# Kernel optimization log

Measured on AMD Instinct MI355X. Metric: run time of the kernel, lower is better.

Reference implementation:

```python
import jax, jax.numpy as jnp
import numpy as np


def setup_inputs() -> dict:
    key = jax.random.key(0)
    ks = jax.random.split(key, 9)
    D, DK, DV = 512, 64, 64
    B, S = 4, 4096
    sd = 1.0 / np.sqrt(D).astype(np.float32)
    so = 1.0 / np.sqrt(DV).astype(np.float32)
    return {
        "x": jax.random.normal(ks[0], (B, S, D), dtype=jnp.float32),
        "Wq": jax.random.normal(ks[1], (D, DK), dtype=jnp.float32) * sd,
        "bq": jnp.zeros((DK,), dtype=jnp.float32),
        "Wk": jax.random.normal(ks[2], (D, DK), dtype=jnp.float32) * sd,
        "bk": jnp.zeros((DK,), dtype=jnp.float32),
        "Wv": jax.random.normal(ks[3], (D, DV), dtype=jnp.float32) * sd,
        "bv": jnp.zeros((DV,), dtype=jnp.float32),
        "Wo": jax.random.normal(ks[4], (DV, D), dtype=jnp.float32) * so,
        "bo": jnp.zeros((D,), dtype=jnp.float32),
    }


def reference(x, Wq, bq, Wk, bk, Wv, bv, Wo, bo):
    # x: (B, S, D)
    B, S, D = x.shape
    dk = Wq.shape[1]
    q = x @ Wq + bq            # (B, S, dk)
    k = x @ Wk + bk            # (B, S, dk)
    v = x @ Wv + bv            # (B, S, dv)
    scores = jnp.einsum("bik,bjk->bij", q, k) / jnp.sqrt(jnp.float32(dk))  # (B,S,S)
    # causal mask: True where j <= i (keep)
    causal = jnp.tril(jnp.ones((S, S), dtype=bool))
    scores = jnp.where(causal[None, :, :], scores, -jnp.inf)
    weights = jax.nn.softmax(scores, axis=-1)   # every row has >=1 unmasked entry
    out = jnp.einsum("bij,bjv->biv", weights, v)  # (B, S, dv)
    return out @ Wo + bo
```

## Files before the change

### kernel.cpp

```cpp
#include <hip/hip_runtime.h>
#include <hip/hip_bf16.h>

#define S_LEN 4096
#define D_MODEL 512
#define DKV 64
#define B_N 4
#define STR 72
#define VSTR 136

typedef __hip_bfloat16 bf16;
typedef __attribute__((ext_vector_type(8))) short short8;
typedef __attribute__((ext_vector_type(4))) float floatx4;

#define MFMA(a, b, c) __builtin_amdgcn_mfma_f32_16x16x32_bf16(a, b, c, 0, 0, 0)

__device__ __forceinline__ float b2f(bf16 v) { return __bfloat162float(v); }

__device__ __forceinline__ unsigned short f2bits(float v) {
    union { bf16 h; unsigned short u; } cv;
    cv.h = __float2bfloat16(v);
    return cv.u;
}
__device__ __forceinline__ float bits2f(unsigned short u) {
    union { bf16 h; unsigned short u; } cv;
    cv.u = u;
    return b2f(cv.h);
}

__global__ __launch_bounds__(64) void detect_kernel(const void* x, int* flag) {
    const int lane = threadIdx.x;
    const bf16* xb = (const bf16*)x;
    int bad = 0;
    for (int k = lane; k < 4096; k += 64) {
        float v = fabsf(b2f(xb[2 * k]));
        if (!(v < 64.f)) bad++;
    }
    #pragma unroll
    for (int off = 32; off >= 1; off >>= 1) bad += __shfl_xor(bad, off);
    if (lane == 0) *flag = (bad > 100) ? 1 : 0;
}

__global__ __launch_bounds__(512) void wprep_kernel(
    const void* __restrict__ Wq, const void* __restrict__ bq,
    const void* __restrict__ Wk, const void* __restrict__ bk,
    const void* __restrict__ Wv, const void* __restrict__ bv,
    const void* __restrict__ Wo, const void* __restrict__ bo,
    bf16* __restrict__ Wfh, bf16* __restrict__ Wfl, float* __restrict__ ball,
    bf16* __restrict__ WoFh, bf16* __restrict__ WoFl, float* __restrict__ ball2,
    const int* __restrict__ flag)
{
    __shared__ float xs[16][513];
    const int blk = blockIdx.x;
    const int tid = threadIdx.x;
    const int f32 = *flag;
    union Pack8 { uint4 u; unsigned short s[8]; };

    if (blk < 12) {
        const int ct = blk;
        const int c0 = ct * 16;
        const int g = c0 >> 6;
        const int cc0 = c0 & 63;
        const void* W    = (g == 0) ? Wq : (g == 1) ? Wk : Wv;
        const void* bias = (g == 0) ? bq : (g == 1) ? bk : bv;

        #pragma unroll
        for (int i = 0; i < 16; ++i) {
            const int idx = tid + 512 * i;
            const int d = idx >> 4, j = idx & 15;
            const float v = f32 ? ((const float*)W)[(size_t)d * DKV + cc0 + j]
                                : b2f(((const bf16*)W)[(size_t)d * DKV + cc0 + j]);
            xs[j][d] = v;
        }
        __syncthreads();

        #pragma unroll
        for (int rep = 0; rep < 2; ++rep) {
            const int f = tid + rep * 512;
            const int kt = f >> 6, lane = f & 63;
            const int quad = lane >> 4, l15 = lane & 15;
            Pack8 ph, pl;
            #pragma unroll
            for (int j = 0; j < 8; ++j) {
                const float v = xs[l15][kt * 32 + quad * 8 + j];
                const unsigned short hb = f2bits(v);
                ph.s[j] = hb;
                pl.s[j] = f2bits(v - bits2f(hb));
            }
            const size_t o = (((size_t)ct * 16 + kt) * 64 + lane) * 8;
            *(uint4*)&Wfh[o] = ph.u;
            *(uint4*)&Wfl[o] = pl.u;
        }
        if (tid < 16)
            ball[c0 + tid] = f32 ? ((const float*)bias)[cc0 + tid]
                                 : b2f(((const bf16*)bias)[cc0 + tid]);
    } else {
        const int ctile = blk - 12;
        const int c0 = ctile * 16;

        #pragma unroll
        for (int rep = 0; rep < 2; ++rep) {
            const int idx = tid + rep * 512;
            const int d = idx >> 4, j = idx & 15;
            const float v = f32 ? ((const float*)Wo)[(size_t)d * D_MODEL + c0 + j]
                                : b2f(((const bf16*)Wo)[(size_t)d * D_MODEL + c0 + j]);
            xs[j][d] = v;
        }
        __syncthreads();

        if (tid < 128) {
            const int kc = tid >> 6, lane = tid & 63;
            const int quad = lane >> 4, l15 = lane & 15;
            Pack8 ph, pl;
            #pragma unroll
            for (int j = 0; j < 8; ++j) {
                const float v = xs[l15][kc * 32 + quad * 8 + j];
                const unsigned short hb = f2bits(v);
                ph.s[j] = hb;
                pl.s[j] = f2bits(v - bits2f(hb));
            }
            const size_t o = (((size_t)ctile * 2 + kc) * 64 + lane) * 8;
            *(uint4*)&WoFh[o] = ph.u;
            *(uint4*)&WoFl[o] = pl.u;
        }
        if (tid < 16)
            ball2[c0 + tid] = f32 ? ((const float*)bo)[c0 + tid]
                                  : b2f(((const bf16*)bo)[c0 + tid]);
    }
}

__global__ __launch_bounds__(512) void qkv_mfma(
    const void* __restrict__ x,
    const bf16* __restrict__ Wfh, const bf16* __restrict__ Wfl,
    const float* __restrict__ ball,
    bf16* __restrict__ Qb, bf16* __restrict__ Kb, bf16* __restrict__ Vt,
    const int* __restrict__ flag)
{
    __shared__ unsigned short hiA[32 * D_MODEL];
    __shared__ unsigned short loA[32 * D_MODEL];
    const int tid = threadIdx.x;
    const int rowBase = blockIdx.x * 32;
    const int f32 = *flag;

    union Pack8 { uint4 u; unsigned short s[8]; };
    if (f32) {
        const float* xr = (const float*)x + (size_t)rowBase * D_MODEL;
        #pragma unroll
        for (int i = 0; i < 4; ++i) {
            const int idx = tid + 512 * i;
            const int r = idx >> 6;
            const int c0 = (idx & 63) << 3;
            const float4 v0 = *(const float4*)&xr[r * D_MODEL + c0];
            const float4 v1 = *(const float4*)&xr[r * D_MODEL + c0 + 4];
            const float vv[8] = {v0.x, v0.y, v0.z, v0.w, v1.x, v1.y, v1.z, v1.w};
            Pack8 ph, pl;
            #pragma unroll
            for (int j = 0; j < 8; ++j) {
                const unsigned short hb = f2bits(vv[j]);
                ph.s[j] = hb;
                pl.s[j] = f2bits(vv[j] - bits2f(hb));
            }
            const int boff = (c0 * 2) ^ ((r & 7) << 4);
            *(uint4*)((char*)hiA + r * 1024 + boff) = ph.u;
            *(uint4*)((char*)loA + r * 1024 + boff) = pl.u;
        }
    } else {
        const unsigned short* xr = (const unsigned short*)x + (size_t)rowBase * D_MODEL;
        #pragma unroll
        for (int i = 0; i < 4; ++i) {
            const int idx = tid + 512 * i;
            const int r = idx >> 6;
            const int c0 = (idx & 63) << 3;
            const uint4 hv = *(const uint4*)&xr[r * D_MODEL + c0];
            const int boff = (c0 * 2) ^ ((r & 7) << 4);
            *(uint4*)((char*)hiA + r * 1024 + boff) = hv;
        }
    }
    __syncthreads();

    const int lane = tid & 63;
    const int w    = tid >> 6;
    const int quad = lane >> 4;
    const int l15  = lane & 15;
    const int wr   = w & 1;
    const int wq   = w >> 1;
    const int arow = wr * 16 + l15;
    const char* hib = (const char*)hiA + arow * 1024;
    const char* lob = (const char*)loA + arow * 1024;
    const int swz = (arow & 7) << 4;

    floatx4 acc[3];
    #pragma unroll
    for (int ct = 0; ct < 3; ++ct) acc[ct] = (floatx4){0.f, 0.f, 0.f, 0.f};

    if (f32) {
        for (int kt = 0; kt < 16; ++kt) {
            const int boff = (kt * 64 + quad * 16) ^ swz;
            const short8 ah = *(const short8*)(hib + boff);
            const short8 al = *(const short8*)(lob + boff);
            #pragma unroll
            for (int ct = 0; ct < 3; ++ct) {
                const size_t fo = (((size_t)(wq * 3 + ct) * 16 + kt) * 64 + lane) * 8;
                const short8 bh = *(const short8*)&Wfh[fo];
                const short8 bl = *(const short8*)&Wfl[fo];
                acc[ct] = MFMA(ah, bh, acc[ct]);
                acc[ct] = MFMA(ah, bl, acc[ct]);
                acc[ct] = MFMA(al, bh, acc[ct]);
            }
        }
    } else {
        for (int kt = 0; kt < 16; ++kt) {
            const int boff = (kt * 64 + quad * 16) ^ swz;
            const short8 ah = *(const short8*)(hib + boff);
            #pragma unroll
            for (int ct = 0; ct < 3; ++ct) {
                const size_t fo = (((size_t)(wq * 3 + ct) * 16 + kt) * 64 + lane) * 8;
                const short8 bh = *(const short8*)&Wfh[fo];
                acc[ct] = MFMA(ah, bh, acc[ct]);
            }
        }
    }

    #pragma unroll
    for (int ct = 0; ct < 3; ++ct) {
        const int gc = wq * 48 + ct * 16 + l15;
        const float bias = ball[gc];
        const float scale = (gc < 64) ? 0.18033688f : 1.0f;
        #pragma unroll
        for (int r = 0; r < 4; ++r) {
            const int gr = rowBase + wr * 16 + quad * 4 + r;
            const bf16 o = __float2bfloat16((acc[ct][r] + bias) * scale);
            if (gc < 64)       Qb[(size_t)gr * DKV + gc] = o;
            else if (gc < 128) Kb[(size_t)gr * DKV + (gc - 64)] = o;
            else {
                const int bb = gr >> 12, sidx = gr & (S_LEN - 1);
                Vt[((size_t)bb * DKV + (gc - 128)) * S_LEN + sidx] = o;
            }
        }
    }
}

__global__ __launch_bounds__(512, 2) void attn_mfma(
    const bf16* __restrict__ Qg, const bf16* __restrict__ Kg,
    const bf16* __restrict__ Vtg, float* __restrict__ Op,
    float* __restrict__ Mp, float* __restrict__ Lp, const int NS)
{
    const int bid = blockIdx.x;
    const int xcd = bid & 7;
    const int rest = bid >> 3;
    const int b   = xcd >> 1;
    const int khH = (NS == 4) ? (rest & 1) : 0;
    const int t   = 31 - ((NS == 4) ? (rest >> 1) : rest);
    const int kh  = khH * 2 + (xcd & 1);
    const int rowBase = t * 128;
    const int tid = threadIdx.x;
    const int lane = tid & 63;
    const int w  = tid >> 6;
    const int quad = lane >> 4;
    const int l15  = lane & 15;

    __shared__ bf16 Kl[128 * STR];
    __shared__ bf16 Vl[64 * VSTR];
    __shared__ bf16 Pl[128 * VSTR];

    const bf16* Qb = Qg + ((size_t)b * S_LEN + rowBase) * DKV;
    const bf16* Kb = Kg + (size_t)b * S_LEN * DKV;
    const bf16* Vb = Vtg + (size_t)b * DKV * S_LEN;

    {
        const int qr = tid >> 2, qd = (tid & 3) * 16;
        *(uint4*)&Pl[qr * VSTR + qd]     = *(const uint4*)&Qb[qr * DKV + qd];
        *(uint4*)&Pl[qr * VSTR + qd + 8] = *(const uint4*)&Qb[qr * DKV + qd + 8];
    }
    __syncthreads();
    short8 qf0, qf1;
    {
        const int qoff = (w * 16 + l15) * VSTR + quad * 8;
        qf0 = *(const short8*)&Pl[qoff];
        qf1 = *(const short8*)&Pl[qoff + 32];
    }

    const short s1b = (short)0x3F80;
    const short8 ones = {s1b, s1b, s1b, s1b, s1b, s1b, s1b, s1b};

    floatx4 acc[4];
    #pragma unroll
    for (int v = 0; v < 4; ++v) acc[v] = (floatx4){0.f, 0.f, 0.f, 0.f};
    floatx4 accl = {0.f, 0.f, 0.f, 0.f};
    float m_run[4];
    #pragma unroll
    for (int r = 0; r < 4; ++r) m_run[r] = -1e30f;

    const int kbMax = t;
    const int kk = tid >> 2, dk = (tid & 3) * 16;
    const int vd = tid >> 3, vk = (tid & 7) * 16;

    uint4 kr0, kr1, vr0, vr1;
    int kb = kh;
    if (kb <= kbMax) {
        const uint4* ks = (const uint4*)&Kb[((size_t)(kb * 128 + kk)) * DKV + dk];
        kr0 = ks[0]; kr1 = ks[1];
        const uint4* vs = (const uint4*)&Vb[(size_t)vd * S_LEN + kb * 128 + vk];
        vr0 = vs[0]; vr1 = vs[1];
    }

    for (; kb <= kbMax; kb += NS) {
        __syncthreads();
        {
            uint4* kd = (uint4*)&Kl[kk * STR + dk];
            kd[0] = kr0; kd[1] = kr1;
            uint4* vdst = (uint4*)&Vl[vd * VSTR + vk];
            vdst[0] = vr0; vdst[1] = vr1;
        }
        __syncthreads();
        if (kb + NS <= kbMax) {
            const uint4* ks = (const uint4*)&Kb[((size_t)((kb + NS) * 128 + kk)) * DKV + dk];
            kr0 = ks[0]; kr1 = ks[1];
            const uint4* vs = (const uint4*)&Vb[(size_t)vd * S_LEN + (kb + NS) * 128 + vk];
            vr0 = vs[0]; vr1 = vs[1];
        }

        floatx4 s[8];
        #pragma unroll
        for (int jt = 0; jt < 8; ++jt) s[jt] = (floatx4){0.f, 0.f, 0.f, 0.f};
        {
            const int qk = quad * 8;
            #pragma unroll
            for (int jt = 0; jt < 8; ++jt) {
                const int kc = (jt * 16 + l15) * STR + qk;
                const short8 ba = *(const short8*)&Kl[kc];
                const short8 bb = *(const short8*)&Kl[kc + 32];
                s[jt] = MFMA(qf0, ba, s[jt]);
                s[jt] = MFMA(qf1, bb, s[jt]);
            }
        }
        if (kb == kbMax) {
            const int rowg = rowBase + w * 16 + quad * 4;
            #pragma unroll
            for (int jt = 0; jt < 8; ++jt) {
                const int kg = kb * 128 + jt * 16 + l15;
                #pragma unroll
                for (int r = 0; r < 4; ++r)
                    if (kg > rowg + r) s[jt][r] = -1e30f;
            }
        }
        float m4[4];
        #pragma unroll
        for (int r = 0; r < 4; ++r) {
            float mm = s[0][r];
            #pragma unroll
            for (int jt = 1; jt < 8; ++jt) mm = fmaxf(mm, s[jt][r]);
            m4[r] = mm;
        }
        #pragma unroll
        for (int off = 1; off < 16; off <<= 1) {
            #pragma unroll
            for (int r = 0; r < 4; ++r) m4[r] = fmaxf(m4[r], __shfl_xor(m4[r], off));
        }
        float alpha[4];
        #pragma unroll
        for (int r = 0; r < 4; ++r) {
            const float mnew = fmaxf(m_run[r], m4[r]);
            alpha[r] = exp2f(m_run[r] - mnew);
            m_run[r] = mnew;
        }
        #pragma unroll
        for (int r = 0; r < 4; ++r) {
            accl[r] *= alpha[r];
            #pragma unroll
            for (int v = 0; v < 4; ++v) acc[v][r] *= alpha[r];
            const int poff = (w * 16 + quad * 4 + r) * VSTR + l15;
            #pragma unroll
            for (int jt = 0; jt < 8; ++jt) {
                const float pp = exp2f(s[jt][r] - m_run[r]);
                Pl[poff + jt * 16] = __float2bfloat16(pp);
            }
        }
        asm volatile("s_waitcnt lgkmcnt(0)" ::: "memory");

        {
            const int pk = quad * 8;
            const int prow = (w * 16 + l15) * VSTR;
            short8 pa[4];
            #pragma unroll
            for (int c = 0; c < 4; ++c)
                pa[c] = *(const short8*)&Pl[prow + pk + c * 32];
            #pragma unroll
            for (int c = 0; c < 4; ++c) accl = MFMA(pa[c], ones, accl);
            #pragma unroll
            for (int v = 0; v < 4; ++v) {
                const int vrow = (v * 16 + l15) * VSTR;
                #pragma unroll
                for (int c = 0; c < 4; ++c) {
                    const short8 vb = *(const short8*)&Vl[vrow + pk + c * 32];
                    acc[v] = MFMA(pa[c], vb, acc[v]);
                }
            }
        }
    }
    #pragma unroll
    for (int r = 0; r < 4; ++r) {
        const int row = rowBase + w * 16 + quad * 4 + r;
        float* op = Op + (((size_t)kh * B_N + b) * S_LEN + row) * DKV + l15;
        #pragma unroll
        for (int v = 0; v < 4; ++v) op[v * 16] = acc[v][r];
    }
    if (l15 == 0) {
        #pragma unroll
        for (int r = 0; r < 4; ++r) {
            const int row = rowBase + w * 16 + quad * 4 + r;
            const size_t mi = ((size_t)kh * B_N + b) * S_LEN + row;
            Mp[mi] = m_run[r];
            Lp[mi] = accl[r];
        }
    }
}

#define PSTR 72
__global__ __launch_bounds__(512) void proj_mfma(
    const float* __restrict__ Op, const float* __restrict__ Mp,
    const float* __restrict__ Lp, const int NS,
    const bf16* __restrict__ WoFh, const bf16* __restrict__ WoFl,
    const float* __restrict__ ball2, void* __restrict__ out,
    const int* __restrict__ flag)
{
    __shared__ unsigned short Ah[32 * PSTR], Al[32 * PSTR];
    const int tid = threadIdx.x;
    const int rowBase = blockIdx.x * 32;
    const int f32 = *flag;

    {
        const int rr = tid >> 4, dd = (tid & 15) * 4;
        const int row = rowBase + rr;
        const size_t part = (size_t)B_N * S_LEN;
        float m = -1e30f;
        #pragma unroll 4
        for (int i = 0; i < NS; ++i) m = fmaxf(m, Mp[i * part + row]);
        float denom = 0.f;
        float oacc[4] = {0.f, 0.f, 0.f, 0.f};
        #pragma unroll 4
        for (int i = 0; i < NS; ++i) {
            const float wi = exp2f(Mp[i * part + row] - m);
            denom += Lp[i * part + row] * wi;
            const float4 v = *(const float4*)&Op[(i * part + row) * DKV + dd];
            oacc[0] += v.x * wi; oacc[1] += v.y * wi;
            oacc[2] += v.z * wi; oacc[3] += v.w * wi;
        }
        const float inv = 1.0f / denom;
        union Pack4 { uint2 u; unsigned short s[4]; };
        Pack4 ph, pl;
        #pragma unroll
        for (int j = 0; j < 4; ++j) {
            const float o = oacc[j] * inv;
            ph.s[j] = f2bits(o);
            pl.s[j] = f2bits(o - bits2f(ph.s[j]));
        }
        *(uint2*)&Ah[rr * PSTR + dd] = ph.u;
        *(uint2*)&Al[rr * PSTR + dd] = pl.u;
    }
    __syncthreads();

    const int lane = tid & 63;
    const int w    = tid >> 6;
    const int quad = lane >> 4;
    const int l15  = lane & 15;
    const int wr   = w & 1;
    const int wcq  = w >> 1;

    const int aoff = (wr * 16 + l15) * PSTR + quad * 8;
    const short8 ah0 = *(const short8*)&Ah[aoff];
    const short8 ah1 = *(const short8*)&Ah[aoff + 32];
    const short8 al0 = *(const short8*)&Al[aoff];
    const short8 al1 = *(const short8*)&Al[aoff + 32];

    floatx4 acc[8];
    #pragma unroll
    for (int ct = 0; ct < 8; ++ct) acc[ct] = (floatx4){0.f, 0.f, 0.f, 0.f};

    if (f32) {
        #pragma unroll
        for (int ct = 0; ct < 8; ++ct) {
            const int ctile = wcq * 8 + ct;
            const size_t o0 = (((size_t)ctile * 2 + 0) * 64 + lane) * 8;
            const size_t o1 = (((size_t)ctile * 2 + 1) * 64 + lane) * 8;
            const short8 bh0 = *(const short8*)&WoFh[o0];
            const short8 bh1 = *(const short8*)&WoFh[o1];
            const short8 bl0 = *(const short8*)&WoFl[o0];
            const short8 bl1 = *(const short8*)&WoFl[o1];
            acc[ct] = MFMA(ah0, bh0, acc[ct]);
            acc[ct] = MFMA(ah1, bh1, acc[ct]);
            acc[ct] = MFMA(ah0, bl0, acc[ct]);
            acc[ct] = MFMA(ah1, bl1, acc[ct]);
            acc[ct] = MFMA(al0, bh0, acc[ct]);
            acc[ct] = MFMA(al1, bh1, acc[ct]);
        }
        float* outf = (float*)out;
        #pragma unroll
        for (int ct = 0; ct < 8; ++ct) {
            const int col = wcq * 128 + ct * 16 + l15;
            const float bias = ball2[col];
            #pragma unroll
            for (int r = 0; r < 4; ++r) {
                const int row = rowBase + wr * 16 + quad * 4 + r;
                outf[(size_t)row * D_MODEL + col] = acc[ct][r] + bias;
            }
        }
    } else {
        #pragma unroll
        for (int ct = 0; ct < 8; ++ct) {
            const int ctile = wcq * 8 + ct;
            const size_t o0 = (((size_t)ctile * 2 + 0) * 64 + lane) * 8;
            const size_t o1 = (((size_t)ctile * 2 + 1) * 64 + lane) * 8;
            const short8 bh0 = *(const short8*)&WoFh[o0];
            const short8 bh1 = *(const short8*)&WoFh[o1];
            acc[ct] = MFMA(ah0, bh0, acc[ct]);
            acc[ct] = MFMA(ah1, bh1, acc[ct]);
            acc[ct] = MFMA(al0, bh0, acc[ct]);
            acc[ct] = MFMA(al1, bh1, acc[ct]);
        }
        bf16* outb = (bf16*)out;
        #pragma unroll
        for (int ct = 0; ct < 8; ++ct) {
            const int col = wcq * 128 + ct * 16 + l15;
            const float bias = ball2[col];
            #pragma unroll
            for (int r = 0; r < 4; ++r) {
                const int row = rowBase + wr * 16 + quad * 4 + r;
                outb[(size_t)row * D_MODEL + col] = __float2bfloat16(acc[ct][r] + bias);
            }
        }
    }
}

extern "C" void kernel_launch(void* const* d_in, const int* in_sizes, int n_in,
                              void* d_out, int out_size, void* d_ws, size_t ws_size,
                              hipStream_t stream) {
    const void* x  = d_in[0];
    const void* Wq = d_in[1];
    const void* bq = d_in[2];
    const void* Wk = d_in[3];
    const void* bk = d_in[4];
    const void* Wv = d_in[5];
    const void* bv = d_in[6];
    const void* Wo = d_in[7];
    const void* bo = d_in[8];

    const int rows = B_N * S_LEN;
    const int NS = (ws_size >= (size_t)30 * 1024 * 1024) ? 4 : 2;

    char* p = (char*)d_ws;
    int*  flag = (int*)p;                          p += 256;
    bf16* Qb = (bf16*)p;                           p += (size_t)rows * DKV * 2;
    bf16* Kb = (bf16*)p;                           p += (size_t)rows * DKV * 2;
    bf16* Vt = (bf16*)p;                           p += (size_t)rows * DKV * 2;
    bf16* Wfh = (bf16*)p;                          p += (size_t)12 * 16 * 64 * 8 * 2;
    bf16* Wfl = (bf16*)p;                          p += (size_t)12 * 16 * 64 * 8 * 2;
    float* ball = (float*)p;                       p += 1024;
    bf16* WoFh = (bf16*)p;                         p += (size_t)32 * 2 * 64 * 8 * 2;
    bf16* WoFl = (bf16*)p;                         p += (size_t)32 * 2 * 64 * 8 * 2;
    float* ball2 = (float*)p;                      p += D_MODEL * 4;
    float* Op = (float*)p;                         p += (size_t)NS * rows * DKV * 4;
    float* Mp = (float*)p;                         p += (size_t)NS * rows * 4;
    float* Lp = (float*)p;                         p += (size_t)NS * rows * 4;

    detect_kernel<<<1, 64, 0, stream>>>(x, flag);
    wprep_kernel<<<44, 512, 0, stream>>>(Wq, bq, Wk, bk, Wv, bv, Wo, bo,
                                         Wfh, Wfl, ball, WoFh, WoFl, ball2, flag);
    qkv_mfma<<<512, 512, 0, stream>>>(x, Wfh, Wfl, ball, Qb, Kb, Vt, flag);
    attn_mfma<<<128 * NS, 512, 0, stream>>>(Qb, Kb, Vt, Op, Mp, Lp, NS);
    proj_mfma<<<512, 512, 0, stream>>>(Op, Mp, Lp, NS, WoFh, WoFl, ball2, d_out, flag);
}
```

Measured before the change: 169.9 us.

## Fuse split-KV merge and output projection into attention via atomic tickets

Removes the separate projection kernel. Each attention block bumps a per-tile atomic ticket after writing its partial O, M and L. The last split block to finish for a 128-row tile merges the partials and runs the Wo projection in four 32-row chunks. This saves one kernel launch and lets projection work overlap with attention blocks that are still running, but only one block per tile does the projection, which serialises that tail work. It also adds shared memory to the attention kernel, which may lower occupancy.

```diff
diff --git a/kernel.cpp b/kernel.cpp
--- a/kernel.cpp
+++ b/kernel.cpp
@@ -7,6 +7,7 @@
 #define B_N 4
 #define STR 72
 #define VSTR 136
+#define PSTR 72
 
 typedef __hip_bfloat16 bf16;
 typedef __attribute__((ext_vector_type(8))) short short8;
@@ -27,8 +28,10 @@
     return b2f(cv.h);
 }
 
-__global__ __launch_bounds__(64) void detect_kernel(const void* x, int* flag) {
+__global__ __launch_bounds__(64) void detect_kernel(const void* x, int* flag,
+                                                    int* tickets) {
     const int lane = threadIdx.x;
+    for (int i = lane; i < 128; i += 64) tickets[i] = 0;
     const bf16* xb = (const bf16*)x;
     int bad = 0;
     for (int k = lane; k < 4096; k += 64) {
@@ -242,7 +245,11 @@
 __global__ __launch_bounds__(512, 2) void attn_mfma(
     const bf16* __restrict__ Qg, const bf16* __restrict__ Kg,
     const bf16* __restrict__ Vtg, float* __restrict__ Op,
-    float* __restrict__ Mp, float* __restrict__ Lp, const int NS)
+    float* __restrict__ Mp, float* __restrict__ Lp, const int NS,
+    int* __restrict__ tickets,
+    const bf16* __restrict__ WoFh, const bf16* __restrict__ WoFl,
+    const float* __restrict__ ball2, void* __restrict__ out,
+    const int* __restrict__ flag)
 {
     const int bid = blockIdx.x;
     const int xcd = bid & 7;
@@ -261,6 +268,8 @@
     __shared__ bf16 Kl[128 * STR];
     __shared__ bf16 Vl[64 * VSTR];
     __shared__ bf16 Pl[128 * VSTR];
+    __shared__ unsigned short Ah[32 * PSTR], Al[32 * PSTR];
+    __shared__ int lastFlag;
 
     const bf16* Qb = Qg + ((size_t)b * S_LEN + rowBase) * DKV;
     const bf16* Kb = Kg + (size_t)b * S_LEN * DKV;
@@ -413,121 +422,118 @@
             Lp[mi] = accl[r];
         }
     }
-}
-
-#define PSTR 72
-__global__ __launch_bounds__(512) void proj_mfma(
-    const float* __restrict__ Op, const float* __restrict__ Mp,
-    const float* __restrict__ Lp, const int NS,
-    const bf16* __restrict__ WoFh, const bf16* __restrict__ WoFl,
-    const float* __restrict__ ball2, void* __restrict__ out,
-    const int* __restrict__ flag)
-{
-    __shared__ unsigned short Ah[32 * PSTR], Al[32 * PSTR];
-    const int tid = threadIdx.x;
-    const int rowBase = blockIdx.x * 32;
+
+    __threadfence();
+    __syncthreads();
+    if (tid == 0) {
+        const int gid = b * 32 + t;
+        const int old = atomicAdd(&tickets[gid], 1);
+        lastFlag = (old == NS - 1);
+    }
+    __syncthreads();
+    if (!lastFlag) return;
+    __threadfence();
+
     const int f32 = *flag;
-
-    {
-        const int rr = tid >> 4, dd = (tid & 15) * 4;
-        const int row = rowBase + rr;
-        const size_t part = (size_t)B_N * S_LEN;
-        float m = -1e30f;
-        #pragma unroll 4
-        for (int i = 0; i < NS; ++i) m = fmaxf(m, Mp[i * part + row]);
-        float denom = 0.f;
-        float oacc[4] = {0.f, 0.f, 0.f, 0.f};
-        #pragma unroll 4
-        for (int i = 0; i < NS; ++i) {
-            const float wi = exp2f(Mp[i * part + row] - m);
-            denom += Lp[i * part + row] * wi;
-            const float4 v = *(const float4*)&Op[(i * part + row) * DKV + dd];
-            oacc[0] += v.x * wi; oacc[1] += v.y * wi;
-            oacc[2] += v.z * wi; oacc[3] += v.w * wi;
-        }
-        const float inv = 1.0f / denom;
-        union Pack4 { uint2 u; unsigned short s[4]; };
-        Pack4 ph, pl;
-        #pragma unroll
-        for (int j = 0; j < 4; ++j) {
-            const float o = oacc[j] * inv;
-            ph.s[j] = f2bits(o);
-            pl.s[j] = f2bits(o - bits2f(ph.s[j]));
-        }
-        *(uint2*)&Ah[rr * PSTR + dd] = ph.u;
-        *(uint2*)&Al[rr * PSTR + dd] = pl.u;
-    }
-    __syncthreads();
-
-    const int lane = tid & 63;
-    const int w    = tid >> 6;
-    const int quad = lane >> 4;
-    const int l15  = lane & 15;
-    const int wr   = w & 1;
-    const int wcq  = w >> 1;
-
-    const int aoff = (wr * 16 + l15) * PSTR + quad * 8;
-    const short8 ah0 = *(const short8*)&Ah[aoff];
-    const short8 ah1 = *(const short8*)&Ah[aoff + 32];
-    const short8 al0 = *(const short8*)&Al[aoff];
-    const short8 al1 = *(const short8*)&Al[aoff + 32];
-
-    floatx4 acc[8];
-    #pragma unroll
-    for (int ct = 0; ct < 8; ++ct) acc[ct] = (floatx4){0.f, 0.f, 0.f, 0.f};
-
-    if (f32) {
-        #pragma unroll
-        for (int ct = 0; ct < 8; ++ct) {
-            const int ctile = wcq * 8 + ct;
-            const size_t o0 = (((size_t)ctile * 2 + 0) * 64 + lane) * 8;
-            const size_t o1 = (((size_t)ctile * 2 + 1) * 64 + lane) * 8;
-            const short8 bh0 = *(const short8*)&WoFh[o0];
-            const short8 bh1 = *(const short8*)&WoFh[o1];
-            const short8 bl0 = *(const short8*)&WoFl[o0];
-            const short8 bl1 = *(const short8*)&WoFl[o1];
-            acc[ct] = MFMA(ah0, bh0, acc[ct]);
-            acc[ct] = MFMA(ah1, bh1, acc[ct]);
-            acc[ct] = MFMA(ah0, bl0, acc[ct]);
-            acc[ct] = MFMA(ah1, bl1, acc[ct]);
-            acc[ct] = MFMA(al0, bh0, acc[ct]);
-            acc[ct] = MFMA(al1, bh1, acc[ct]);
-        }
-        float* outf = (float*)out;
-        #pragma unroll
-        for (int ct = 0; ct < 8; ++ct) {
-            const int col = wcq * 128 + ct * 16 + l15;
-            const float bias = ball2[col];
-            #pragma unroll
-            for (int r = 0; r < 4; ++r) {
-                const int row = rowBase + wr * 16 + quad * 4 + r;
-                outf[(size_t)row * D_MODEL + col] = acc[ct][r] + bias;
-            }
-        }
-    } else {
-        #pragma unroll
-        for (int ct = 0; ct < 8; ++ct) {
-            const int ctile = wcq * 8 + ct;
-            const size_t o0 = (((size_t)ctile * 2 + 0) * 64 + lane) * 8;
-            const size_t o1 = (((size_t)ctile * 2 + 1) * 64 + lane) * 8;
-            const short8 bh0 = *(const short8*)&WoFh[o0];
-            const short8 bh1 = *(const short8*)&WoFh[o1];
-            acc[ct] = MFMA(ah0, bh0, acc[ct]);
-            acc[ct] = MFMA(ah1, bh1, acc[ct]);
-            acc[ct] = MFMA(al0, bh0, acc[ct]);
-            acc[ct] = MFMA(al1, bh1, acc[ct]);
-        }
-        bf16* outb = (bf16*)out;
-        #pragma unroll
-        for (int ct = 0; ct < 8; ++ct) {
-            const int col = wcq * 128 + ct * 16 + l15;
-            const float bias = ball2[col];
-            #pragma unroll
-            for (int r = 0; r < 4; ++r) {
-                const int row = rowBase + wr * 16 + quad * 4 + r;
-                outb[(size_t)row * D_MODEL + col] = __float2bfloat16(acc[ct][r] + bias);
-            }
-        }
+    const int wr  = w & 1;
+    const int wcq = w >> 1;
+    for (int cb = 0; cb < 4; ++cb) {
+        const int grow0 = b * S_LEN + rowBase + cb * 32;
+        {
+            const int rr = tid >> 4, dd = (tid & 15) * 4;
+            const int row = grow0 + rr;
+            const size_t part = (size_t)B_N * S_LEN;
+            float m = -1e30f;
+            #pragma unroll 4
+            for (int i = 0; i < NS; ++i) m = fmaxf(m, Mp[i * part + row]);
+            float denom = 0.f;
+            float oacc[4] = {0.f, 0.f, 0.f, 0.f};
+            #pragma unroll 4
+            for (int i = 0; i < NS; ++i) {
+                const float wi = exp2f(Mp[i * part + row] - m);
+                denom += Lp[i * part + row] * wi;
+                const float4 v = *(const float4*)&Op[(i * part + row) * DKV + dd];
+                oacc[0] += v.x * wi; oacc[1] += v.y * wi;
+                oacc[2] += v.z * wi; oacc[3] += v.w * wi;
+            }
+            const float inv = 1.0f / denom;
+            union Pack4 { uint2 u; unsigned short s[4]; };
+            Pack4 ph, pl;
+            #pragma unroll
+            for (int j = 0; j < 4; ++j) {
+                const float o = oacc[j] * inv;
+                ph.s[j] = f2bits(o);
+                pl.s[j] = f2bits(o - bits2f(ph.s[j]));
+            }
+            *(uint2*)&Ah[rr * PSTR + dd] = ph.u;
+            *(uint2*)&Al[rr * PSTR + dd] = pl.u;
+        }
+        __syncthreads();
+
+        const int aoff = (wr * 16 + l15) * PSTR + quad * 8;
+        const short8 ah0 = *(const short8*)&Ah[aoff];
+        const short8 ah1 = *(const short8*)&Ah[aoff + 32];
+        const short8 al0 = *(const short8*)&Al[aoff];
+        const short8 al1 = *(const short8*)&Al[aoff + 32];
+
+        floatx4 pacc[8];
+        #pragma unroll
+        for (int ct = 0; ct < 8; ++ct) pacc[ct] = (floatx4){0.f, 0.f, 0.f, 0.f};
+
+        if (f32) {
+            #pragma unroll
+            for (int ct = 0; ct < 8; ++ct) {
+                const int ctile = wcq * 8 + ct;
+                const size_t o0 = (((size_t)ctile * 2 + 0) * 64 + lane) * 8;
+                const size_t o1 = (((size_t)ctile * 2 + 1) * 64 + lane) * 8;
+                const short8 bh0 = *(const short8*)&WoFh[o0];
+                const short8 bh1 = *(const short8*)&WoFh[o1];
+                const short8 bl0 = *(const short8*)&WoFl[o0];
+                const short8 bl1 = *(const short8*)&WoFl[o1];
+                pacc[ct] = MFMA(ah0, bh0, pacc[ct]);
+                pacc[ct] = MFMA(ah1, bh1, pacc[ct]);
+                pacc[ct] = MFMA(ah0, bl0, pacc[ct]);
+                pacc[ct] = MFMA(ah1, bl1, pacc[ct]);
+                pacc[ct] = MFMA(al0, bh0, pacc[ct]);
+                pacc[ct] = MFMA(al1, bh1, pacc[ct]);
+            }
+            float* outf = (float*)out;
+            #pragma unroll
+            for (int ct = 0; ct < 8; ++ct) {
+                const int col = wcq * 128 + ct * 16 + l15;
+                const float bias = ball2[col];
+                #pragma unroll
+                for (int r = 0; r < 4; ++r) {
+                    const int row = grow0 + wr * 16 + quad * 4 + r;
+                    outf[(size_t)row * D_MODEL + col] = pacc[ct][r] + bias;
+                }
+            }
+        } else {
+            #pragma unroll
+            for (int ct = 0; ct < 8; ++ct) {
+                const int ctile = wcq * 8 + ct;
+                const size_t o0 = (((size_t)ctile * 2 + 0) * 64 + lane) * 8;
+                const size_t o1 = (((size_t)ctile * 2 + 1) * 64 + lane) * 8;
+                const short8 bh0 = *(const short8*)&WoFh[o0];
+                const short8 bh1 = *(const short8*)&WoFh[o1];
+                pacc[ct] = MFMA(ah0, bh0, pacc[ct]);
+                pacc[ct] = MFMA(ah1, bh1, pacc[ct]);
+                pacc[ct] = MFMA(al0, bh0, pacc[ct]);
+                pacc[ct] = MFMA(al1, bh1, pacc[ct]);
+            }
+            bf16* outb = (bf16*)out;
+            #pragma unroll
+            for (int ct = 0; ct < 8; ++ct) {
+                const int col = wcq * 128 + ct * 16 + l15;
+                const float bias = ball2[col];
+                #pragma unroll
+                for (int r = 0; r < 4; ++r) {
+                    const int row = grow0 + wr * 16 + quad * 4 + r;
+                    outb[(size_t)row * D_MODEL + col] = __float2bfloat16(pacc[ct][r] + bias);
+                }
+            }
+        }
+        __syncthreads();
     }
 }
 
@@ -549,6 +555,7 @@
 
     char* p = (char*)d_ws;
     int*  flag = (int*)p;                          p += 256;
+    int*  tickets = (int*)p;                       p += 1024;
     bf16* Qb = (bf16*)p;                           p += (size_t)rows * DKV * 2;
     bf16* Kb = (bf16*)p;                           p += (size_t)rows * DKV * 2;
     bf16* Vt = (bf16*)p;                           p += (size_t)rows * DKV * 2;
@@ -562,10 +569,10 @@
     float* Mp = (float*)p;                         p += (size_t)NS * rows * 4;
     float* Lp = (float*)p;                         p += (size_t)NS * rows * 4;
 
-    detect_kernel<<<1, 64, 0, stream>>>(x, flag);
+    detect_kernel<<<1, 64, 0, stream>>>(x, flag, tickets);
     wprep_kernel<<<44, 512, 0, stream>>>(Wq, bq, Wk, bk, Wv, bv, Wo, bo,
                                          Wfh, Wfl, ball, WoFh, WoFl, ball2, flag);
     qkv_mfma<<<512, 512, 0, stream>>>(x, Wfh, Wfl, ball, Qb, Kb, Vt, flag);
-    attn_mfma<<<128 * NS, 512, 0, stream>>>(Qb, Kb, Vt, Op, Mp, Lp, NS);
-    proj_mfma<<<512, 512, 0, stream>>>(Op, Mp, Lp, NS, WoFh, WoFl, ball2, d_out, flag);
-}
+    attn_mfma<<<128 * NS, 512, 0, stream>>>(Qb, Kb, Vt, Op, Mp, Lp, NS, tickets,
+                                            WoFh, WoFl, ball2, d_out, flag);
+}
```

Measured after the change: 340.1 us. 2x slower.

## Split causal attention into fixed two-block chunks and fold detect into wprep

Applied to the files above, without the earlier changes.

Attention work is repartitioned so each block handles at most two key blocks for one query tile, giving 272 work items per batch (1088 blocks) instead of a fixed NS-way interleaved split. Per-tile partial outputs go to slot-indexed buffers, and proj_mfma merges a variable number of partials per row. This is meant to balance the triangular causal workload and shorten per-block latency. In exchange it writes and reads many more partial O/M/L buffers, which adds memory traffic and merge cost. The separate detect kernel launch is also folded into wprep, with each block recomputing the input-format flag itself.

```diff
diff --git a/kernel.cpp b/kernel.cpp
--- a/kernel.cpp
+++ b/kernel.cpp
@@ -27,33 +27,41 @@
     return b2f(cv.h);
 }
 
-__global__ __launch_bounds__(64) void detect_kernel(const void* x, int* flag) {
-    const int lane = threadIdx.x;
-    const bf16* xb = (const bf16*)x;
-    int bad = 0;
-    for (int k = lane; k < 4096; k += 64) {
-        float v = fabsf(b2f(xb[2 * k]));
-        if (!(v < 64.f)) bad++;
-    }
-    #pragma unroll
-    for (int off = 32; off >= 1; off >>= 1) bad += __shfl_xor(bad, off);
-    if (lane == 0) *flag = (bad > 100) ? 1 : 0;
-}
+#define NSLOT_B 272
+__device__ __forceinline__ int offT(int t) { return (t * t + 2 * t + (t & 1)) >> 2; }
 
 __global__ __launch_bounds__(512) void wprep_kernel(
+    const void* __restrict__ x,
     const void* __restrict__ Wq, const void* __restrict__ bq,
     const void* __restrict__ Wk, const void* __restrict__ bk,
     const void* __restrict__ Wv, const void* __restrict__ bv,
     const void* __restrict__ Wo, const void* __restrict__ bo,
     bf16* __restrict__ Wfh, bf16* __restrict__ Wfl, float* __restrict__ ball,
     bf16* __restrict__ WoFh, bf16* __restrict__ WoFl, float* __restrict__ ball2,
-    const int* __restrict__ flag)
+    int* __restrict__ flag)
 {
     __shared__ float xs[16][513];
+    __shared__ int sflag;
     const int blk = blockIdx.x;
     const int tid = threadIdx.x;
-    const int f32 = *flag;
     union Pack8 { uint4 u; unsigned short s[8]; };
+
+    if (tid < 64) {
+        const bf16* xb = (const bf16*)x;
+        int bad = 0;
+        for (int k = tid; k < 4096; k += 64) {
+            float v = fabsf(b2f(xb[2 * k]));
+            if (!(v < 64.f)) bad++;
+        }
+        #pragma unroll
+        for (int off = 32; off >= 1; off >>= 1) bad += __shfl_xor(bad, off);
+        if (tid == 0) {
+            sflag = (bad > 100) ? 1 : 0;
+            if (blk == 0) *flag = sflag;
+        }
+    }
+    __syncthreads();
+    const int f32 = sflag;
 
     if (blk < 12) {
         const int ct = blk;
@@ -242,15 +250,19 @@
 __global__ __launch_bounds__(512, 2) void attn_mfma(
     const bf16* __restrict__ Qg, const bf16* __restrict__ Kg,
     const bf16* __restrict__ Vtg, float* __restrict__ Op,
-    float* __restrict__ Mp, float* __restrict__ Lp, const int NS)
+    float* __restrict__ Mp, float* __restrict__ Lp)
 {
     const int bid = blockIdx.x;
-    const int xcd = bid & 7;
-    const int rest = bid >> 3;
-    const int b   = xcd >> 1;
-    const int khH = (NS == 4) ? (rest & 1) : 0;
-    const int t   = 31 - ((NS == 4) ? (rest >> 1) : rest);
-    const int kh  = khH * 2 + (xcd & 1);
+    const int b = bid & 3;
+    const int j = (NSLOT_B - 1) - (bid >> 2);
+    int t = (int)(2.0f * sqrtf((float)j + 1.0f));
+    if (t > 31) t = 31;
+    while (offT(t) > j) --t;
+    while (t < 31 && offT(t + 1) <= j) ++t;
+    const int p = j - offT(t);
+    const int kb0 = 2 * p;
+    const int kb1 = min(2 * p + 1, t);
+    const int slot = b * NSLOT_B + offT(t) + p;
     const int rowBase = t * 128;
     const int tid = threadIdx.x;
     const int lane = tid & 63;
@@ -290,20 +302,18 @@
     #pragma unroll
     for (int r = 0; r < 4; ++r) m_run[r] = -1e30f;
 
-    const int kbMax = t;
     const int kk = tid >> 2, dk = (tid & 3) * 16;
     const int vd = tid >> 3, vk = (tid & 7) * 16;
 
     uint4 kr0, kr1, vr0, vr1;
-    int kb = kh;
-    if (kb <= kbMax) {
-        const uint4* ks = (const uint4*)&Kb[((size_t)(kb * 128 + kk)) * DKV + dk];
+    {
+        const uint4* ks = (const uint4*)&Kb[((size_t)(kb0 * 128 + kk)) * DKV + dk];
         kr0 = ks[0]; kr1 = ks[1];
-        const uint4* vs = (const uint4*)&Vb[(size_t)vd * S_LEN + kb * 128 + vk];
+        const uint4* vs = (const uint4*)&Vb[(size_t)vd * S_LEN + kb0 * 128 + vk];
         vr0 = vs[0]; vr1 = vs[1];
     }
 
-    for (; kb <= kbMax; kb += NS) {
+    for (int kb = kb0; kb <= kb1; ++kb) {
         __syncthreads();
         {
             uint4* kd = (uint4*)&Kl[kk * STR + dk];
@@ -312,10 +322,10 @@
             vdst[0] = vr0; vdst[1] = vr1;
         }
         __syncthreads();
-        if (kb + NS <= kbMax) {
-            const uint4* ks = (const uint4*)&Kb[((size_t)((kb + NS) * 128 + kk)) * DKV + dk];
+        if (kb + 1 <= kb1) {
+            const uint4* ks = (const uint4*)&Kb[((size_t)((kb + 1) * 128 + kk)) * DKV + dk];
             kr0 = ks[0]; kr1 = ks[1];
-            const uint4* vs = (const uint4*)&Vb[(size_t)vd * S_LEN + (kb + NS) * 128 + vk];
+            const uint4* vs = (const uint4*)&Vb[(size_t)vd * S_LEN + (kb + 1) * 128 + vk];
             vr0 = vs[0]; vr1 = vs[1];
         }
 
@@ -333,7 +343,7 @@
                 s[jt] = MFMA(qf1, bb, s[jt]);
             }
         }
-        if (kb == kbMax) {
+        if (kb == t) {
             const int rowg = rowBase + w * 16 + quad * 4;
             #pragma unroll
             for (int jt = 0; jt < 8; ++jt) {
@@ -399,18 +409,17 @@
     }
     #pragma unroll
     for (int r = 0; r < 4; ++r) {
-        const int row = rowBase + w * 16 + quad * 4 + r;
-        float* op = Op + (((size_t)kh * B_N + b) * S_LEN + row) * DKV + l15;
+        const int lrow = w * 16 + quad * 4 + r;
+        float* op = Op + ((size_t)slot * 128 + lrow) * DKV + l15;
         #pragma unroll
         for (int v = 0; v < 4; ++v) op[v * 16] = acc[v][r];
     }
     if (l15 == 0) {
         #pragma unroll
         for (int r = 0; r < 4; ++r) {
-            const int row = rowBase + w * 16 + quad * 4 + r;
-            const size_t mi = ((size_t)kh * B_N + b) * S_LEN + row;
-            Mp[mi] = m_run[r];
-            Lp[mi] = accl[r];
+            const int lrow = w * 16 + quad * 4 + r;
+            Mp[slot * 128 + lrow] = m_run[r];
+            Lp[slot * 128 + lrow] = accl[r];
         }
     }
 }
@@ -418,7 +427,7 @@
 #define PSTR 72
 __global__ __launch_bounds__(512) void proj_mfma(
     const float* __restrict__ Op, const float* __restrict__ Mp,
-    const float* __restrict__ Lp, const int NS,
+    const float* __restrict__ Lp,
     const bf16* __restrict__ WoFh, const bf16* __restrict__ WoFl,
     const float* __restrict__ ball2, void* __restrict__ out,
     const int* __restrict__ flag)
@@ -431,17 +440,22 @@
     {
         const int rr = tid >> 4, dd = (tid & 15) * 4;
         const int row = rowBase + rr;
-        const size_t part = (size_t)B_N * S_LEN;
+        const int bb = row >> 12;
+        const int sIdx = row & (S_LEN - 1);
+        const int tt = sIdx >> 7;
+        const int lrow = sIdx & 127;
+        const int nparts = (tt + 2) >> 1;
+        const int sbase = bb * NSLOT_B + offT(tt);
+
         float m = -1e30f;
-        #pragma unroll 4
-        for (int i = 0; i < NS; ++i) m = fmaxf(m, Mp[i * part + row]);
+        for (int i = 0; i < nparts; ++i)
+            m = fmaxf(m, Mp[(sbase + i) * 128 + lrow]);
         float denom = 0.f;
         float oacc[4] = {0.f, 0.f, 0.f, 0.f};
-        #pragma unroll 4
-        for (int i = 0; i < NS; ++i) {
-            const float wi = exp2f(Mp[i * part + row] - m);
-            denom += Lp[i * part + row] * wi;
-            const float4 v = *(const float4*)&Op[(i * part + row) * DKV + dd];
+        for (int i = 0; i < nparts; ++i) {
+            const float wi = exp2f(Mp[(sbase + i) * 128 + lrow] - m);
+            denom += Lp[(sbase + i) * 128 + lrow] * wi;
+            const float4 v = *(const float4*)&Op[((size_t)(sbase + i) * 128 + lrow) * DKV + dd];
             oacc[0] += v.x * wi; oacc[1] += v.y * wi;
             oacc[2] += v.z * wi; oacc[3] += v.w * wi;
         }
@@ -449,10 +463,10 @@
         union Pack4 { uint2 u; unsigned short s[4]; };
         Pack4 ph, pl;
         #pragma unroll
-        for (int j = 0; j < 4; ++j) {
-            const float o = oacc[j] * inv;
-            ph.s[j] = f2bits(o);
-            pl.s[j] = f2bits(o - bits2f(ph.s[j]));
+        for (int jj = 0; jj < 4; ++jj) {
+            const float o = oacc[jj] * inv;
+            ph.s[jj] = f2bits(o);
+            pl.s[jj] = f2bits(o - bits2f(ph.s[jj]));
         }
         *(uint2*)&Ah[rr * PSTR + dd] = ph.u;
         *(uint2*)&Al[rr * PSTR + dd] = pl.u;
@@ -545,7 +559,7 @@
     const void* bo = d_in[8];
 
     const int rows = B_N * S_LEN;
-    const int NS = (ws_size >= (size_t)30 * 1024 * 1024) ? 4 : 2;
+    const int nslots = B_N * NSLOT_B;
 
     char* p = (char*)d_ws;
     int*  flag = (int*)p;                          p += 256;
@@ -558,14 +572,13 @@
     bf16* WoFh = (bf16*)p;                         p += (size_t)32 * 2 * 64 * 8 * 2;
     bf16* WoFl = (bf16*)p;                         p += (size_t)32 * 2 * 64 * 8 * 2;
     float* ball2 = (float*)p;                      p += D_MODEL * 4;
-    float* Op = (float*)p;                         p += (size_t)NS * rows * DKV * 4;
-    float* Mp = (float*)p;                         p += (size_t)NS * rows * 4;
-    float* Lp = (float*)p;                         p += (size_t)NS * rows * 4;
-
-    detect_kernel<<<1, 64, 0, stream>>>(x, flag);
-    wprep_kernel<<<44, 512, 0, stream>>>(Wq, bq, Wk, bk, Wv, bv, Wo, bo,
+    float* Op = (float*)p;                         p += (size_t)nslots * 128 * DKV * 4;
+    float* Mp = (float*)p;                         p += (size_t)nslots * 128 * 4;
+    float* Lp = (float*)p;                         p += (size_t)nslots * 128 * 4;
+
+    wprep_kernel<<<44, 512, 0, stream>>>(x, Wq, bq, Wk, bk, Wv, bv, Wo, bo,
                                          Wfh, Wfl, ball, WoFh, WoFl, ball2, flag);
     qkv_mfma<<<512, 512, 0, stream>>>(x, Wfh, Wfl, ball, Qb, Kb, Vt, flag);
-    attn_mfma<<<128 * NS, 512, 0, stream>>>(Qb, Kb, Vt, Op, Mp, Lp, NS);
-    proj_mfma<<<512, 512, 0, stream>>>(Op, Mp, Lp, NS, WoFh, WoFl, ball2, d_out, flag);
-}
+    attn_mfma<<<nslots, 512, 0, stream>>>(Qb, Kb, Vt, Op, Mp, Lp);
+    proj_mfma<<<512, 512, 0, stream>>>(Op, Mp, Lp, WoFh, WoFl, ball2, d_out, flag);
+}
```

Result: faster. 164.3 us (-3.3%).
